# Kernel optimization log

Measured on AMD Instinct MI355X. Metric: run time of the kernel, lower is better.

The kernel has to match this reference:

```python
import jax, jax.numpy as jnp
import numpy as np

N_NODES = 100000
N_EDGES = 600000
H_FEATS = 128


def setup_inputs() -> dict:
    key = jax.random.key(0)
    k_h, k_src, k_dst, k_w1, k_w2 = jax.random.split(key, 5)
    h = jax.random.normal(k_h, (N_NODES, H_FEATS), dtype=jnp.float32)
    src = jax.random.randint(k_src, (N_EDGES,), 0, N_NODES, dtype=jnp.int64)
    dst = jax.random.randint(k_dst, (N_EDGES,), 0, N_NODES, dtype=jnp.int64)
    # torch.nn.Linear-style params: out = x @ W.T + b
    W1_w = jax.random.normal(k_w1, (H_FEATS, 2 * H_FEATS), dtype=jnp.float32) * (1.0 / np.sqrt(2 * H_FEATS))
    W1_b = jnp.zeros((H_FEATS,), dtype=jnp.float32)
    W2_w = jax.random.normal(k_w2, (1, H_FEATS), dtype=jnp.float32) * (1.0 / np.sqrt(H_FEATS))
    W2_b = jnp.zeros((1,), dtype=jnp.float32)
    return {"h": h, "src": src, "dst": dst, "W1_w": W1_w, "W1_b": W1_b, "W2_w": W2_w, "W2_b": W2_b}


def reference(h, src, dst, W1_w, W1_b, W2_w, W2_b):
    # Gather endpoint features per edge and concatenate: [E, 2*h_feats]
    edge_feat = jnp.concatenate([h[src], h[dst]], axis=-1)
    # 2-layer MLP per edge: Linear -> ReLU -> Linear, scalar score per edge
    hid = jax.nn.relu(edge_feat @ W1_w.T + W1_b)  # [E, h_feats]
    score = hid @ W2_w.T + W2_b                   # [E, 1]
    return score[:, 0]                            # [E]
```

## Files before the change

kernel.cpp:

```cpp
#include <hip/hip_runtime.h>
#include <hip/hip_bf16.h>
#include <stdint.h>

typedef short bf16x8 __attribute__((ext_vector_type(8)));
typedef float f32x4  __attribute__((ext_vector_type(4)));

__device__ __forceinline__ ushort f2b(float f) {
  __hip_bfloat16 t = __float2bfloat16(f);
  return *reinterpret_cast<ushort*>(&t);
}
__device__ __forceinline__ bf16x8 pack8(float4 a, float4 b) {
  bf16x8 r;
  r[0]=(short)f2b(a.x); r[1]=(short)f2b(a.y); r[2]=(short)f2b(a.z); r[3]=(short)f2b(a.w);
  r[4]=(short)f2b(b.x); r[5]=(short)f2b(b.y); r[6]=(short)f2b(b.z); r[7]=(short)f2b(b.w);
  return r;
}

__global__ void repack_W1(const float* __restrict__ W1, int4* __restrict__ blob) {
  const int tid = blockIdx.x * 256 + threadIdx.x;
  const int l15  = tid & 15;
  const int lg   = (tid >> 4) & 3;
  const int kk   = (tid >> 6) & 3;
  const int nt   = (tid >> 8) & 7;
  const int half = (tid >> 11) & 1;
  const float* wp = W1 + (size_t)(nt * 16 + l15) * 256 + half * 128 + kk * 32 + lg * 8;
  const float4 fa = *(const float4*)wp;
  const float4 fb = *(const float4*)(wp + 4);
  bf16x8 r = pack8(fa, fb);
  blob[tid] = *reinterpret_cast<int4*>(&r);
}

__global__ __launch_bounds__(256, 4) void node_uv(
    const float* __restrict__ h, const int4* __restrict__ blob,
    const float* __restrict__ b1,
    uint8_t* __restrict__ u8, uint8_t* __restrict__ v8,
    float* __restrict__ su, float* __restrict__ sv,
    int Nn, int NT, int nblocks, int niter)
{
  __shared__ ushort As[2048];

  const int t0   = threadIdx.x;
  const int w    = t0 >> 6;
  const int l    = t0 & 63;
  const int l15  = l & 15;
  const int lg   = l >> 4;
  const int half = w >> 1;
  const int hw   = w & 1;

  bf16x8 bfrag[4][4];
#pragma unroll
  for (int ntl = 0; ntl < 4; ++ntl)
#pragma unroll
    for (int kk = 0; kk < 4; ++kk) {
      int4 x = blob[((half * 8 + hw * 4 + ntl) * 4 + kk) * 64 + l];
      bfrag[ntl][kk] = *reinterpret_cast<bf16x8*>(&x);
    }

  float b1r[4];
#pragma unroll
  for (int ntl = 0; ntl < 4; ++ntl)
    b1r[ntl] = half ? 0.f : b1[hw * 64 + ntl * 16 + l15];

  uint8_t* __restrict__ outp = half ? v8 : u8;
  float*   __restrict__ outs = half ? sv : su;

  const float4* h4 = (const float4*)h;

  int t = blockIdx.x;
  if (t < NT) {
    const size_t hb = (size_t)t * 512;
#pragma unroll
    for (int k = 0; k < 2; ++k) {
      const int i = k * 256 + t0, row = i >> 5, c = i & 31;
      const int gr = t * 16 + row;
      float4 g = h4[gr < Nn ? hb + i : 0];
      ushort4 o; o.x = f2b(g.x); o.y = f2b(g.y); o.z = f2b(g.z); o.w = f2b(g.w);
      *(ushort4*)(As + row * 128 + (((c >> 1) ^ (row & 7)) << 3) + (c & 1) * 4) = o;
    }
  }
  __syncthreads();

  for (int it = 0; it < niter; ++it) {
    const int tn = t + nblocks;

    float4 g[2];
    if (tn < NT) {
      const size_t hb = (size_t)tn * 512;
#pragma unroll
      for (int k = 0; k < 2; ++k) {
        const int i = k * 256 + t0;
        const int gr = tn * 16 + (i >> 5);
        g[k] = h4[gr < Nn ? hb + i : 0];
      }
    }

    if (t < NT) {
      f32x4 acc[4];
#pragma unroll
      for (int ntl = 0; ntl < 4; ++ntl) acc[ntl] = (f32x4){0.f, 0.f, 0.f, 0.f};

#pragma unroll
      for (int kk = 0; kk < 4; ++kk) {
        const int slot = (kk * 4 + lg) ^ (l15 & 7);
        int4 av = *(const int4*)(As + l15 * 128 + slot * 8);
        const bf16x8 a = *reinterpret_cast<bf16x8*>(&av);
#pragma unroll
        for (int ntl = 0; ntl < 4; ++ntl)
          acc[ntl] = __builtin_amdgcn_mfma_f32_16x16x32_bf16(a, bfrag[ntl][kk], acc[ntl], 0, 0, 0);
      }

      const int n0 = t * 16;
#pragma unroll
      for (int r = 0; r < 4; ++r) {
        float vals[4];
        float m = 1e-30f;
#pragma unroll
        for (int ntl = 0; ntl < 4; ++ntl) {
          const float x = acc[ntl][r] + b1r[ntl];
          vals[ntl] = x;
          m = fmaxf(m, fabsf(x));
        }
        m = fmaxf(m, __shfl_xor(m, 1));
        m = fmaxf(m, __shfl_xor(m, 2));
        m = fmaxf(m, __shfl_xor(m, 4));
        m = fmaxf(m, __shfl_xor(m, 8));
        const float inv = 127.0f * __builtin_amdgcn_rcpf(m);
        uint32_t pk = 0;
#pragma unroll
        for (int j = 0; j < 4; ++j) {
          const int q = (int)rintf(vals[j] * inv) + 128;
          pk |= (uint32_t)q << (8 * j);
        }
        const int node = n0 + lg * 4 + r;
        if (node < Nn) {
          *(uint32_t*)(outp + (size_t)node * 128 + l15 * 8 + hw * 4) = pk;
          if (l15 == 0) outs[node * 2 + hw] = m * (1.0f / 127.0f);
        }
      }
    }

    __syncthreads();
    if (tn < NT) {
#pragma unroll
      for (int k = 0; k < 2; ++k) {
        const int i = k * 256 + t0, row = i >> 5, c = i & 31;
        ushort4 o; o.x = f2b(g[k].x); o.y = f2b(g[k].y); o.z = f2b(g[k].z); o.w = f2b(g[k].w);
        *(ushort4*)(As + row * 128 + (((c >> 1) ^ (row & 7)) << 3) + (c & 1) * 4) = o;
      }
    }
    __syncthreads();
    t = tn;
  }
}

__global__ __launch_bounds__(256) void edge_score_i8(
    const uint8_t* __restrict__ u8, const uint8_t* __restrict__ v8,
    const float* __restrict__ su, const float* __restrict__ sv,
    const int* __restrict__ src, const int* __restrict__ dst,
    const float* __restrict__ w2, const float* __restrict__ b2p,
    float* __restrict__ out, int E)
{
  const int t  = threadIdx.x;
  const int l  = t & 63;
  const int q  = l & 15;
  const int lg = l >> 4;

  float w2r[8];
#pragma unroll
  for (int j = 0; j < 8; ++j) w2r[j] = w2[j * 16 + q];
  const float b2 = b2p[0];

  const int gw = blockIdx.x * 4 + (t >> 6);
  const int TW = gridDim.x * 4;
  const float2* su2 = (const float2*)su;
  const float2* sv2 = (const float2*)sv;

  for (int base = gw * 16; base < E; base += TW * 16) {
    int e[4]; bool ok[4];
    uint2 ug[4], vg[4];
    float2 ss[4], sd[4];
#pragma unroll
    for (int i = 0; i < 4; ++i) {
      e[i]  = base + i * 4 + lg;
      ok[i] = e[i] < E;
      const int eS = ok[i] ? e[i] : 0;
      const int s = src[eS];
      const int d = dst[eS];
      ug[i] = *(const uint2*)(u8 + (size_t)s * 128 + q * 8);
      vg[i] = *(const uint2*)(v8 + (size_t)d * 128 + q * 8);
      ss[i] = su2[s];
      sd[i] = sv2[d];
    }
#pragma unroll
    for (int i = 0; i < 4; ++i) {
      const uint32_t ux = ug[i].x, uy = ug[i].y;
      const uint32_t vx = vg[i].x, vy = vg[i].y;
      const float bse0 = -128.0f * (ss[i].x + sd[i].x);
      const float bse1 = -128.0f * (ss[i].y + sd[i].y);
      float acc = 0.f;
#pragma unroll
      for (int j = 0; j < 4; ++j) {
        const float cu = (float)((ux >> (8 * j)) & 0xffu);
        const float cv = (float)((vx >> (8 * j)) & 0xffu);
        float x = fmaf(cu, ss[i].x, fmaf(cv, sd[i].x, bse0));
        x = fmaxf(x, 0.f);
        acc = fmaf(x, w2r[j], acc);
      }
#pragma unroll
      for (int j = 0; j < 4; ++j) {
        const float cu = (float)((uy >> (8 * j)) & 0xffu);
        const float cv = (float)((vy >> (8 * j)) & 0xffu);
        float x = fmaf(cu, ss[i].y, fmaf(cv, sd[i].y, bse1));
        x = fmaxf(x, 0.f);
        acc = fmaf(x, w2r[4 + j], acc);
      }
      acc += __shfl_xor(acc, 1);
      acc += __shfl_xor(acc, 2);
      acc += __shfl_xor(acc, 4);
      acc += __shfl_xor(acc, 8);
      if (q == 0 && ok[i]) out[e[i]] = acc + b2;
    }
  }
}

extern "C" void kernel_launch(void* const* d_in, const int* in_sizes, int n_in,
                              void* d_out, int out_size, void* d_ws, size_t ws_size,
                              hipStream_t stream) {
  const float* h   = (const float*)d_in[0];
  const int*   src = (const int*)d_in[1];
  const int*   dst = (const int*)d_in[2];
  const float* W1  = (const float*)d_in[3];
  const float* b1  = (const float*)d_in[4];
  const float* w2  = (const float*)d_in[5];
  const float* b2  = (const float*)d_in[6];
  float* out = (float*)d_out;

  const int nh = in_sizes[0];
  const int Nn = nh / 128;
  const int E  = in_sizes[1];

  uint8_t* ws = (uint8_t*)d_ws;
  int4*  blob = (int4*)ws;
  size_t off  = 65536;
  float* su   = (float*)(ws + off);  off += (size_t)Nn * 8;
  off = (off + 511) & ~(size_t)511;
  float* sv   = (float*)(ws + off);  off += (size_t)Nn * 8;
  off = (off + 511) & ~(size_t)511;
  uint8_t* u8 = ws + off;            off += (size_t)Nn * 128;
  uint8_t* v8 = ws + off;

  hipLaunchKernelGGL(repack_W1, dim3(16), dim3(256), 0, stream, W1, blob);

  const int NT      = (Nn + 15) / 16;
  const int nblocks = 1024;
  const int niter   = (NT + nblocks - 1) / nblocks;
  hipLaunchKernelGGL(node_uv, dim3(nblocks), dim3(256), 0, stream,
                     h, blob, b1, u8, v8, su, sv, Nn, NT, nblocks, niter);

  hipLaunchKernelGGL(edge_score_i8, dim3(2048), dim3(256), 0, stream,
                     u8, v8, su, sv, src, dst, w2, b2, out, E);
}
```

Baseline: 60.17 us.

## Double-buffer node tile LDS with two-ahead prefetch and widen edge batching

The node_uv kernel now keeps two LDS tile buffers and prefetches h two tiles ahead, so each iteration needs one barrier instead of two and global loads overlap more with the MFMA work. Launch bounds drop to 3 blocks per SIMD and the grid shrinks from 1024 to 768 blocks to fit the extra registers and LDS. The edge scoring kernel processes 8 edges per lane group per iteration instead of 4, putting more gathers in flight. The costs are higher register pressure and lower occupancy. Out-of-range prefetches are clamped to row 0 rather than skipped, which wastes some loads.

After: 61.09 us. Within noise of the previous version (+1.5%).

```diff
diff --git a/kernel.cpp b/kernel.cpp
--- a/kernel.cpp
+++ b/kernel.cpp
@@ -30,14 +30,14 @@
   blob[tid] = *reinterpret_cast<int4*>(&r);
 }
 
-__global__ __launch_bounds__(256, 4) void node_uv(
+__global__ __launch_bounds__(256, 3) void node_uv(
     const float* __restrict__ h, const int4* __restrict__ blob,
     const float* __restrict__ b1,
     uint8_t* __restrict__ u8, uint8_t* __restrict__ v8,
     float* __restrict__ su, float* __restrict__ sv,
     int Nn, int NT, int nblocks, int niter)
 {
-  __shared__ ushort As[2048];
+  __shared__ ushort As[2][2048];
 
   const int t0   = threadIdx.x;
   const int w    = t0 >> 6;
@@ -66,35 +66,44 @@
 
   const float4* h4 = (const float4*)h;
 
-  int t = blockIdx.x;
-  if (t < NT) {
-    const size_t hb = (size_t)t * 512;
-#pragma unroll
-    for (int k = 0; k < 2; ++k) {
-      const int i = k * 256 + t0, row = i >> 5, c = i & 31;
-      const int gr = t * 16 + row;
-      float4 g = h4[gr < Nn ? hb + i : 0];
-      ushort4 o; o.x = f2b(g.x); o.y = f2b(g.y); o.z = f2b(g.z); o.w = f2b(g.w);
-      *(ushort4*)(As + row * 128 + (((c >> 1) ^ (row & 7)) << 3) + (c & 1) * 4) = o;
-    }
-  }
+#define LOADT(T, g)                                            \
+  {                                                            \
+    const size_t hb = (size_t)(T) * 512;                       \
+    _Pragma("unroll")                                          \
+    for (int k = 0; k < 2; ++k) {                              \
+      const int i = k * 256 + t0;                              \
+      const int gr = (T) * 16 + (i >> 5);                      \
+      (g)[k] = h4[gr < Nn ? hb + i : 0];                       \
+    }                                                          \
+  }
+
+#define STORET(b, g)                                           \
+  {                                                            \
+    _Pragma("unroll")                                          \
+    for (int k = 0; k < 2; ++k) {                              \
+      const int i = k * 256 + t0, row = i >> 5, c = i & 31;    \
+      ushort4 o;                                               \
+      o.x = f2b((g)[k].x); o.y = f2b((g)[k].y);                \
+      o.z = f2b((g)[k].z); o.w = f2b((g)[k].w);                \
+      *(ushort4*)(&As[b][row * 128 + (((c >> 1) ^ (row & 7)) << 3) + (c & 1) * 4]) = o; \
+    }                                                          \
+  }
+
+  int tc = blockIdx.x;
+  int tn = tc + nblocks;
+  float4 gC[2], gN[2], gNN[2];
+  LOADT(tc, gC);
+  LOADT(tn, gN);
+  STORET(0, gC);
   __syncthreads();
+  int cur = 0;
 
   for (int it = 0; it < niter; ++it) {
-    const int tn = t + nblocks;
-
-    float4 g[2];
-    if (tn < NT) {
-      const size_t hb = (size_t)tn * 512;
-#pragma unroll
-      for (int k = 0; k < 2; ++k) {
-        const int i = k * 256 + t0;
-        const int gr = tn * 16 + (i >> 5);
-        g[k] = h4[gr < Nn ? hb + i : 0];
-      }
-    }
-
-    if (t < NT) {
+    const int tnn = tn + nblocks;
+    LOADT(tnn, gNN);
+    STORET(cur ^ 1, gN);
+
+    if (tc < NT) {
       f32x4 acc[4];
 #pragma unroll
       for (int ntl = 0; ntl < 4; ++ntl) acc[ntl] = (f32x4){0.f, 0.f, 0.f, 0.f};
@@ -102,14 +111,14 @@
 #pragma unroll
       for (int kk = 0; kk < 4; ++kk) {
         const int slot = (kk * 4 + lg) ^ (l15 & 7);
-        int4 av = *(const int4*)(As + l15 * 128 + slot * 8);
+        int4 av = *(const int4*)(&As[cur][l15 * 128 + slot * 8]);
         const bf16x8 a = *reinterpret_cast<bf16x8*>(&av);
 #pragma unroll
         for (int ntl = 0; ntl < 4; ++ntl)
           acc[ntl] = __builtin_amdgcn_mfma_f32_16x16x32_bf16(a, bfrag[ntl][kk], acc[ntl], 0, 0, 0);
       }
 
-      const int n0 = t * 16;
+      const int n0 = tc * 16;
 #pragma unroll
       for (int r = 0; r < 4; ++r) {
         float vals[4];
@@ -140,17 +149,12 @@
     }
 
     __syncthreads();
-    if (tn < NT) {
-#pragma unroll
-      for (int k = 0; k < 2; ++k) {
-        const int i = k * 256 + t0, row = i >> 5, c = i & 31;
-        ushort4 o; o.x = f2b(g[k].x); o.y = f2b(g[k].y); o.z = f2b(g[k].z); o.w = f2b(g[k].w);
-        *(ushort4*)(As + row * 128 + (((c >> 1) ^ (row & 7)) << 3) + (c & 1) * 4) = o;
-      }
-    }
-    __syncthreads();
-    t = tn;
-  }
+    tc = tn; tn = tnn;
+    gN[0] = gNN[0]; gN[1] = gNN[1];
+    cur ^= 1;
+  }
+#undef LOADT
+#undef STORET
 }
 
 __global__ __launch_bounds__(256) void edge_score_i8(
@@ -175,12 +179,12 @@
   const float2* su2 = (const float2*)su;
   const float2* sv2 = (const float2*)sv;
 
-  for (int base = gw * 16; base < E; base += TW * 16) {
-    int e[4]; bool ok[4];
-    uint2 ug[4], vg[4];
-    float2 ss[4], sd[4];
-#pragma unroll
-    for (int i = 0; i < 4; ++i) {
+  for (int base = gw * 32; base < E; base += TW * 32) {
+    int e[8]; bool ok[8];
+    uint2 ug[8], vg[8];
+    float2 ss[8], sd[8];
+#pragma unroll
+    for (int i = 0; i < 8; ++i) {
       e[i]  = base + i * 4 + lg;
       ok[i] = e[i] < E;
       const int eS = ok[i] ? e[i] : 0;
@@ -192,7 +196,7 @@
       sd[i] = sv2[d];
     }
 #pragma unroll
-    for (int i = 0; i < 4; ++i) {
+    for (int i = 0; i < 8; ++i) {
       const uint32_t ux = ug[i].x, uy = ug[i].y;
       const uint32_t vx = vg[i].x, vy = vg[i].y;
       const float bse0 = -128.0f * (ss[i].x + sd[i].x);
@@ -252,7 +256,7 @@
   hipLaunchKernelGGL(repack_W1, dim3(16), dim3(256), 0, stream, W1, blob);
 
   const int NT      = (Nn + 15) / 16;
-  const int nblocks = 1024;
+  const int nblocks = 768;
   const int niter   = (NT + nblocks - 1) / nblocks;
   hipLaunchKernelGGL(node_uv, dim3(nblocks), dim3(256), 0, stream,
                      h, blob, b1, u8, v8, su, sv, Nn, NT, nblocks, niter);
```

## Pipeline node_uv h loads with direct-to-LDS DMA across four buffers

Applied to the files above, without the earlier changes.

The node projection kernel now loads fp32 h tiles straight into LDS with global_load_lds into a 4-deep ring buffer, keeping loads for tiles two iterations ahead in flight. It waits with vmcnt-based barriers and converts to bf16 when reading from LDS. This replaces the register-staged prefetch and the extra barrier-guarded LDS store. Out-of-range rows are clamped and written to padded rows, so workspace buffers grow by 16 rows. The edge kernel grid is also enlarged. The cost is 32KB of LDS per block, which may limit occupancy, and the vmcnt counts are hand-tuned and fragile.

Result: no change. 60.91 us (+1.2%).

```diff
diff --git a/kernel.cpp b/kernel.cpp
--- a/kernel.cpp
+++ b/kernel.cpp
@@ -30,14 +30,20 @@
   blob[tid] = *reinterpret_cast<int4*>(&r);
 }
 
+__device__ __forceinline__ void dma16(const float4* g, void* lds) {
+  __builtin_amdgcn_global_load_lds(
+      (const __attribute__((address_space(1))) uint32_t*)g,
+      (__attribute__((address_space(3))) uint32_t*)lds, 16, 0, 0);
+}
+
 __global__ __launch_bounds__(256, 4) void node_uv(
     const float* __restrict__ h, const int4* __restrict__ blob,
     const float* __restrict__ b1,
     uint8_t* __restrict__ u8, uint8_t* __restrict__ v8,
     float* __restrict__ su, float* __restrict__ sv,
-    int Nn, int NT, int nblocks, int niter)
+    int Nn, int NT, int nb, int niter)
 {
-  __shared__ ushort As[2048];
+  __shared__ uint8_t As[4][8192];
 
   const int t0   = threadIdx.x;
   const int w    = t0 >> 6;
@@ -66,91 +72,98 @@
 
   const float4* h4 = (const float4*)h;
 
-  int t = blockIdx.x;
-  if (t < NT) {
-    const size_t hb = (size_t)t * 512;
-#pragma unroll
-    for (int k = 0; k < 2; ++k) {
-      const int i = k * 256 + t0, row = i >> 5, c = i & 31;
-      const int gr = t * 16 + row;
-      float4 g = h4[gr < Nn ? hb + i : 0];
-      ushort4 o; o.x = f2b(g.x); o.y = f2b(g.y); o.z = f2b(g.z); o.w = f2b(g.w);
-      *(ushort4*)(As + row * 128 + (((c >> 1) ^ (row & 7)) << 3) + (c & 1) * 4) = o;
-    }
-  }
-  __syncthreads();
-
-  for (int it = 0; it < niter; ++it) {
-    const int tn = t + nblocks;
-
-    float4 g[2];
-    if (tn < NT) {
-      const size_t hb = (size_t)tn * 512;
-#pragma unroll
-      for (int k = 0; k < 2; ++k) {
-        const int i = k * 256 + t0;
-        const int gr = tn * 16 + (i >> 5);
-        g[k] = h4[gr < Nn ? hb + i : 0];
-      }
-    }
-
-    if (t < NT) {
-      f32x4 acc[4];
-#pragma unroll
-      for (int ntl = 0; ntl < 4; ++ntl) acc[ntl] = (f32x4){0.f, 0.f, 0.f, 0.f};
-
-#pragma unroll
-      for (int kk = 0; kk < 4; ++kk) {
-        const int slot = (kk * 4 + lg) ^ (l15 & 7);
-        int4 av = *(const int4*)(As + l15 * 128 + slot * 8);
-        const bf16x8 a = *reinterpret_cast<bf16x8*>(&av);
-#pragma unroll
-        for (int ntl = 0; ntl < 4; ++ntl)
-          acc[ntl] = __builtin_amdgcn_mfma_f32_16x16x32_bf16(a, bfrag[ntl][kk], acc[ntl], 0, 0, 0);
-      }
-
-      const int n0 = t * 16;
-#pragma unroll
-      for (int r = 0; r < 4; ++r) {
-        float vals[4];
-        float m = 1e-30f;
-#pragma unroll
-        for (int ntl = 0; ntl < 4; ++ntl) {
-          const float x = acc[ntl][r] + b1r[ntl];
-          vals[ntl] = x;
-          m = fmaxf(m, fabsf(x));
-        }
-        m = fmaxf(m, __shfl_xor(m, 1));
-        m = fmaxf(m, __shfl_xor(m, 2));
-        m = fmaxf(m, __shfl_xor(m, 4));
-        m = fmaxf(m, __shfl_xor(m, 8));
-        const float inv = 127.0f * __builtin_amdgcn_rcpf(m);
-        uint32_t pk = 0;
-#pragma unroll
-        for (int j = 0; j < 4; ++j) {
-          const int q = (int)rintf(vals[j] * inv) + 128;
-          pk |= (uint32_t)q << (8 * j);
-        }
-        const int node = n0 + lg * 4 + r;
-        if (node < Nn) {
-          *(uint32_t*)(outp + (size_t)node * 128 + l15 * 8 + hw * 4) = pk;
-          if (l15 == 0) outs[node * 2 + hw] = m * (1.0f / 127.0f);
-        }
-      }
-    }
-
-    __syncthreads();
-    if (tn < NT) {
-#pragma unroll
-      for (int k = 0; k < 2; ++k) {
-        const int i = k * 256 + t0, row = i >> 5, c = i & 31;
-        ushort4 o; o.x = f2b(g[k].x); o.y = f2b(g[k].y); o.z = f2b(g[k].z); o.w = f2b(g[k].w);
-        *(ushort4*)(As + row * 128 + (((c >> 1) ^ (row & 7)) << 3) + (c & 1) * 4) = o;
-      }
-    }
-    __syncthreads();
-    t = tn;
-  }
+  const int s0 = w * 128 + l,  srow0 = s0 >> 5, sc0 = s0 & 31;
+  const int s1 = s0 + 64,      srow1 = s1 >> 5, sc1 = s1 & 31;
+  const int coff0 = sc0 ^ (srow0 & 7);
+  const int coff1 = sc1 ^ (srow1 & 7);
+
+#define DMA_TILE(T, bi)                                                     \
+  {                                                                         \
+    const int tt = (T) < NT ? (T) : NT - 1;                                 \
+    int gr0 = tt * 16 + srow0; if (gr0 >= Nn) gr0 = Nn - 1;                 \
+    int gr1 = tt * 16 + srow1; if (gr1 >= Nn) gr1 = Nn - 1;                 \
+    dma16(h4 + (size_t)gr0 * 32 + coff0, &As[bi][w * 2048]);                \
+    dma16(h4 + (size_t)gr1 * 32 + coff1, &As[bi][w * 2048 + 1024]);         \
+  }
+
+#define VMBAR(N)                                                            \
+  asm volatile("s_waitcnt vmcnt(" #N ")" ::: "memory");                     \
+  __builtin_amdgcn_sched_barrier(0);                                        \
+  __builtin_amdgcn_s_barrier();                                             \
+  __builtin_amdgcn_sched_barrier(0);
+
+#define COMPUTE(bi, TC)                                                     \
+  if ((TC) < NT) {                                                          \
+    const uint8_t* Ab = &As[bi][0];                                         \
+    f32x4 acc[4];                                                           \
+    _Pragma("unroll")                                                       \
+    for (int ntl = 0; ntl < 4; ++ntl) acc[ntl] = (f32x4){0.f,0.f,0.f,0.f};  \
+    _Pragma("unroll")                                                       \
+    for (int kk = 0; kk < 4; ++kk) {                                        \
+      const int lc  = kk * 8 + lg * 2;                                      \
+      const int pc0 = lc ^ (l15 & 7);                                       \
+      const int pc1 = (lc + 1) ^ (l15 & 7);                                 \
+      const float4 fa = *(const float4*)(Ab + l15 * 512 + pc0 * 16);        \
+      const float4 fb = *(const float4*)(Ab + l15 * 512 + pc1 * 16);        \
+      const bf16x8 a = pack8(fa, fb);                                       \
+      _Pragma("unroll")                                                     \
+      for (int ntl = 0; ntl < 4; ++ntl)                                     \
+        acc[ntl] = __builtin_amdgcn_mfma_f32_16x16x32_bf16(                 \
+            a, bfrag[ntl][kk], acc[ntl], 0, 0, 0);                          \
+    }                                                                       \
+    const int n0 = (TC) * 16;                                               \
+    _Pragma("unroll")                                                       \
+    for (int r = 0; r < 4; ++r) {                                           \
+      float vals[4];                                                        \
+      float m = 1e-30f;                                                     \
+      _Pragma("unroll")                                                     \
+      for (int ntl = 0; ntl < 4; ++ntl) {                                   \
+        const float x = acc[ntl][r] + b1r[ntl];                             \
+        vals[ntl] = x;                                                      \
+        m = fmaxf(m, fabsf(x));                                             \
+      }                                                                     \
+      m = fmaxf(m, __shfl_xor(m, 1));                                       \
+      m = fmaxf(m, __shfl_xor(m, 2));                                       \
+      m = fmaxf(m, __shfl_xor(m, 4));                                       \
+      m = fmaxf(m, __shfl_xor(m, 8));                                       \
+      const float inv = 127.0f * __builtin_amdgcn_rcpf(m);                  \
+      uint32_t pk = 0;                                                      \
+      _Pragma("unroll")                                                     \
+      for (int j = 0; j < 4; ++j) {                                         \
+        const int q = (int)rintf(vals[j] * inv) + 128;                      \
+        pk |= (uint32_t)q << (8 * j);                                       \
+      }                                                                     \
+      const int node = n0 + lg * 4 + r;                                     \
+      const int nd   = node < Nn ? node : Nn;   \
+      *(uint32_t*)(outp + (size_t)nd * 128 + l15 * 8 + hw * 4) = pk;        \
+      if (l15 == 0) outs[nd * 2 + hw] = m * (1.0f / 127.0f);                \
+    }                                                                       \
+  }
+
+  int tc = blockIdx.x;
+  DMA_TILE(tc, 0);
+  DMA_TILE(tc + nb, 1);
+
+  DMA_TILE(tc + 2 * nb, 2);
+  VMBAR(4)
+  COMPUTE(0, tc)
+  tc += nb;
+
+  DMA_TILE(tc + 2 * nb, 3);
+  VMBAR(9)
+  COMPUTE(1, tc)
+  tc += nb;
+
+  for (int it = 2; it < niter; ++it) {
+    DMA_TILE(tc + 2 * nb, (it + 2) & 3);
+    VMBAR(14)
+    const int bi = it & 3;
+    COMPUTE(bi, tc)
+    tc += nb;
+  }
+#undef DMA_TILE
+#undef VMBAR
+#undef COMPUTE
 }
 
 __global__ __launch_bounds__(256) void edge_score_i8(
@@ -242,11 +255,11 @@
   uint8_t* ws = (uint8_t*)d_ws;
   int4*  blob = (int4*)ws;
   size_t off  = 65536;
-  float* su   = (float*)(ws + off);  off += (size_t)Nn * 8;
+  float* su   = (float*)(ws + off);  off += (size_t)(Nn + 16) * 8;
   off = (off + 511) & ~(size_t)511;
-  float* sv   = (float*)(ws + off);  off += (size_t)Nn * 8;
+  float* sv   = (float*)(ws + off);  off += (size_t)(Nn + 16) * 8;
   off = (off + 511) & ~(size_t)511;
-  uint8_t* u8 = ws + off;            off += (size_t)Nn * 128;
+  uint8_t* u8 = ws + off;            off += (size_t)(Nn + 16) * 128;
   uint8_t* v8 = ws + off;
 
   hipLaunchKernelGGL(repack_W1, dim3(16), dim3(256), 0, stream, W1, blob);
@@ -257,6 +270,6 @@
   hipLaunchKernelGGL(node_uv, dim3(nblocks), dim3(256), 0, stream,
                      h, blob, b1, u8, v8, su, sv, Nn, NT, nblocks, niter);
 
-  hipLaunchKernelGGL(edge_score_i8, dim3(2048), dim3(256), 0, stream,
+  hipLaunchKernelGGL(edge_score_i8, dim3(3072), dim3(256), 0, stream,
                      u8, v8, su, sv, src, dst, w2, b2, out, E);
 }
```
